# Optimization experiments

Hardware: AMD Instinct MI355X
Metric: run time of the kernel (lower is better)

Reference implementation:

```python
import jax, jax.numpy as jnp
import numpy as np


def setup_inputs() -> dict:
    key = jax.random.key(0)
    k1, k2, k3 = jax.random.split(key, 3)
    B, Cout, Cin, H, W = 8, 64, 64, 256, 256
    Wf_rfft = W // 2 + 1
    init_scale = 0.1
    x = jax.random.normal(k1, (B, Cout, H, W), dtype=jnp.float32)
    weight_fft = jax.random.normal(k2, (Cout, Cin, H, Wf_rfft), dtype=jnp.float32) * init_scale
    bias = jax.random.normal(k3, (Cin,), dtype=jnp.float32) * init_scale
    return {"x": x, "weight_fft": weight_fft, "bias": bias}


def reference(x, weight_fft, bias):
    # x: (B, Cout, H, W); weight_fft: (Cout, Cin, Hf, Wf_rfft); bias: (Cin,)
    B, Cout, H, W = x.shape
    _, Cin, Hf, Wf_rfft = weight_fft.shape
    X_fft = jnp.fft.rfft2(x, axes=(2, 3))  # (B, Cout, H, W//2+1) complex
    # Channel contraction over Cout per frequency bin (original code does a
    # broadcast multiply-then-sum; einsum computes identical math without
    # materializing the (B,Cout,Cin,Hf,Wf) intermediate).
    Z_fft = jnp.einsum('bohw,oihw->bihw', X_fft, weight_fft.astype(X_fft.dtype))
    real_Wf = 2 * (Wf_rfft - 1) if Wf_rfft > 1 else 1
    y = jnp.fft.irfft2(Z_fft, s=(Hf, real_Wf), axes=(2, 3))
    y = y[..., :H, :W]
    return y + bias[None, :, None, None]
```

## Files before the change

kernel.cpp:

```cpp
#include <hip/hip_runtime.h>
#include <hip/hip_bf16.h>
#include <math.h>

#define PI_F 3.14159265358979323846f


#define NWACT 15

__device__ __forceinline__ unsigned pack_bf(float re, float im) {
    unsigned ur = __float_as_uint(re);
    unsigned ui = __float_as_uint(im);
    ur = (ur + 0x7fffu + ((ur >> 16) & 1u)) >> 16;
    ui = (ui + 0x7fffu + ((ui >> 16) & 1u)) & 0xffff0000u;
    return ur | ui;
}
__device__ __forceinline__ float2 unpack_bf(unsigned p) {
    return make_float2(__uint_as_float(p << 16),
                       __uint_as_float(p & 0xffff0000u));
}

__device__ __forceinline__ int s2i(int p) { return p ^ (((p >> 4) & 3) << 2); }

__device__ __forceinline__ float2 cadd(float2 a, float2 b){ return make_float2(a.x+b.x, a.y+b.y); }
__device__ __forceinline__ float2 csub(float2 a, float2 b){ return make_float2(a.x-b.x, a.y-b.y); }
__device__ __forceinline__ float2 cmul(float2 a, float2 b){ return make_float2(a.x*b.x-a.y*b.y, a.x*b.y+a.y*b.x); }

template<int SGN>
__device__ __forceinline__ void mk_tw(int jt, float invh, float2& w1, float2& w2) {
    const float th = (SGN < 0 ? -PI_F : PI_F) * (float)jt * invh;
    __sincosf(th, &w1.y, &w1.x);
    __sincosf(0.5f * th, &w2.y, &w2.x);
}

template<int SGN>
__device__ __forceinline__ void quad2(float2& u0, float2& u1, float2& u2, float2& u3,
                                      float2 w1, float2 w2) {
    const float2 t1 = cmul(w1, u1), t3 = cmul(w1, u3);
    const float2 v0 = cadd(u0, t1), v1 = csub(u0, t1);
    const float2 v2 = cadd(u2, t3), v3 = csub(u2, t3);
    const float2 t2 = cmul(w2, v2);
    float2 t4 = cmul(w2, v3);
    t4 = (SGN < 0) ? make_float2(t4.y, -t4.x) : make_float2(-t4.y, t4.x);
    u0 = cadd(v0, t2); u2 = csub(v0, t2);
    u1 = cadd(v1, t4); u3 = csub(v1, t4);
}

template<int SGN>
__device__ __forceinline__ void fft256(float2* w, int j, const float2* tw,
                                       float2& o0, float2& o1, float2& o2, float2& o3) {
    const int r = (int)(__brev((unsigned)j) >> 26);
    float2 u0 = w[s2i(r)], u1 = w[s2i(r + 128)], u2 = w[s2i(r + 64)], u3 = w[s2i(r + 192)];
    __builtin_amdgcn_wave_barrier();
    {
        const float2 v0 = cadd(u0, u1), v1 = csub(u0, u1);
        const float2 v2 = cadd(u2, u3), v3 = csub(u2, u3);
        const float2 t4 = (SGN < 0) ? make_float2(v3.y, -v3.x) : make_float2(-v3.y, v3.x);
        u0 = cadd(v0, v2); u2 = csub(v0, v2);
        u1 = cadd(v1, t4); u3 = csub(v1, t4);
    }
    const int p4 = s2i(4 * j);
    *(float4*)&w[p4]     = make_float4(u0.x, u0.y, u1.x, u1.y);
    *(float4*)&w[p4 + 2] = make_float4(u2.x, u2.y, u3.x, u3.y);
    __builtin_amdgcn_wave_barrier();
    {
        const int p = ((j >> 2) << 4) | (j & 3);
        float2 a0 = w[s2i(p)], a1 = w[s2i(p+4)], a2 = w[s2i(p+8)], a3 = w[s2i(p+12)];
        quad2<SGN>(a0, a1, a2, a3, tw[0], tw[1]);
        w[s2i(p)] = a0; w[s2i(p+4)] = a1; w[s2i(p+8)] = a2; w[s2i(p+12)] = a3;
    }
    __builtin_amdgcn_wave_barrier();
    {
        const int p = ((j >> 4) << 6) | (j & 15);
        float2 a0 = w[s2i(p)], a1 = w[s2i(p+16)], a2 = w[s2i(p+32)], a3 = w[s2i(p+48)];
        quad2<SGN>(a0, a1, a2, a3, tw[2], tw[3]);
        w[s2i(p)] = a0; w[s2i(p+16)] = a1; w[s2i(p+32)] = a2; w[s2i(p+48)] = a3;
    }
    __builtin_amdgcn_wave_barrier();
    {
        float2 a0 = w[s2i(j)], a1 = w[s2i(j+64)], a2 = w[s2i(j+128)], a3 = w[s2i(j+192)];
        quad2<SGN>(a0, a1, a2, a3, tw[4], tw[5]);
        o0 = a0; o1 = a1; o2 = a2; o3 = a3;
    }
}

#define SMEM_BYTES (132096 + NWACT * 256 * 8)

__global__ __launch_bounds__(1024) void k_fwd2d(const float* __restrict__ x,
                                                unsigned* __restrict__ Xf) {
    extern __shared__ char smem[];
    unsigned* S = (unsigned*)smem;
    float2* w = (float2*)(smem + 132096) + ((threadIdx.x >> 6) << 8);
    const int t = threadIdx.x, f = t >> 6, j = t & 63;
    const int bo = blockIdx.x;
    const float* xi = x + (size_t)bo * 65536;

    float2 tw[6];
    mk_tw<-1>(j & 3,  0.25f,       tw[0], tw[1]);
    mk_tw<-1>(j & 15, 1.0f/16.0f,  tw[2], tw[3]);
    mk_tw<-1>(j,      1.0f/64.0f,  tw[4], tw[5]);

    if (f < NWACT) {
        for (int rp = f; rp < 128; rp += NWACT) {
            const int r1 = rp, r2 = rp + 128;
            const float4 va = ((const float4*)(xi + (r1 << 8)))[j];
            const float4 vb = ((const float4*)(xi + (r2 << 8)))[j];
            const int p4 = s2i(4 * j);
            *(float4*)&w[p4]     = make_float4(va.x, vb.x, va.y, vb.y);
            *(float4*)&w[p4 + 2] = make_float4(va.z, vb.z, va.w, vb.w);
            __builtin_amdgcn_wave_barrier();
            float2 o0, o1, o2, o3;
            fft256<-1>(w, j, tw, o0, o1, o2, o3);
            const int src = (64 - j) & 63;
            float2 P3, P2;
            P3.x = __shfl(o3.x, src); P3.y = __shfl(o3.y, src);
            P2.x = __shfl(o2.x, src); P2.y = __shfl(o2.y, src);
            const float2 Cj = (j == 0) ? make_float2(o0.x, -o0.y)
                                       : make_float2(P3.x, -P3.y);
            const float2 Ck = (j == 0) ? make_float2(P3.x, -P3.y)
                                       : make_float2(P2.x, -P2.y);
            const float2 Aj = make_float2(0.5f * (o0.x + Cj.x), 0.5f * (o0.y + Cj.y));
            const float2 Bj = make_float2(0.5f * (o0.y - Cj.y), -0.5f * (o0.x - Cj.x));
            const float2 Ak = make_float2(0.5f * (o1.x + Ck.x), 0.5f * (o1.y + Ck.y));
            const float2 Bk = make_float2(0.5f * (o1.y - Ck.y), -0.5f * (o1.x - Ck.x));
            S[r1 * 129 + j]      = pack_bf(Aj.x, Aj.y);
            S[r1 * 129 + 64 + j] = pack_bf(Ak.x, Ak.y);
            S[r2 * 129 + j]      = pack_bf(Bj.x, Bj.y);
            S[r2 * 129 + 64 + j] = pack_bf(Bk.x, Bk.y);
            if (j == 0) {
                S[r1 * 129 + 128] = pack_bf(o2.x, 0.0f);
                S[r2 * 129 + 128] = pack_bf(o2.y, 0.0f);
            }
            __builtin_amdgcn_wave_barrier();
        }
    }
    __syncthreads();
    if (f < NWACT) {
        for (int c = f; c <= 128; c += NWACT) {
#pragma unroll
            for (int k = 0; k < 4; ++k)
                w[s2i(j + 64 * k)] = unpack_bf(S[(j + 64 * k) * 129 + c]);
            __builtin_amdgcn_wave_barrier();
            float2 o0, o1, o2, o3;
            fft256<-1>(w, j, tw, o0, o1, o2, o3);
            S[(j      ) * 129 + c] = pack_bf(o0.x, o0.y);
            S[(j +  64) * 129 + c] = pack_bf(o1.x, o1.y);
            S[(j + 128) * 129 + c] = pack_bf(o2.x, o2.y);
            S[(j + 192) * 129 + c] = pack_bf(o3.x, o3.y);
            __builtin_amdgcn_wave_barrier();
        }
    }
    __syncthreads();
    uint4* dst = (uint4*)(Xf + (size_t)bo * 33024);
    const uint4* src4 = (const uint4*)S;
    for (int e = t; e < 8256; e += 1024) dst[e] = src4[e];
}

__global__ __launch_bounds__(256) void k_einsum(unsigned* __restrict__ Xf,
                                                const float* __restrict__ Wt) {
    __shared__ unsigned xs[512][32];
    const int t = threadIdx.x;
    const int bid = blockIdx.x;
    const int nid = (bid & 7) * 129 + (bid >> 3);
    const size_t n0 = (size_t)nid * 32;

#pragma unroll
    for (int k = 0; k < 16; ++k) {
        const int e = t + 256 * k;
        const int pr = e >> 3, q = e & 7;
        const uint4 v = *reinterpret_cast<const uint4*>(
            Xf + (size_t)pr * 33024 + n0 + (q << 2));
        *reinterpret_cast<uint4*>(&xs[pr][q << 2]) = v;
    }
    __syncthreads();

    const int nl = t & 31, j = t >> 5;
    float2 acc[8][8];
#pragma unroll
    for (int r = 0; r < 8; ++r)
#pragma unroll
        for (int b = 0; b < 8; ++b) acc[r][b] = make_float2(0.0f, 0.0f);

    const float* Wb = Wt + n0 + nl;
    auto wload = [&](int o, float (&buf)[8]) {
#pragma unroll
        for (int r = 0; r < 8; ++r)
            buf[r] = __builtin_nontemporal_load(
                Wb + (size_t)((o << 6) | ((r << 3) | j)) * 33024);
    };
    auto fmab = [&](int o, const float (&wc)[8]) {
        float2 xv[8];
#pragma unroll
        for (int b = 0; b < 8; ++b) xv[b] = unpack_bf(xs[(b << 6) | o][nl]);
#pragma unroll
        for (int r = 0; r < 8; ++r)
#pragma unroll
            for (int b = 0; b < 8; ++b) {
                acc[r][b].x += xv[b].x * wc[r];
                acc[r][b].y += xv[b].y * wc[r];
            }
    };

    float wA[8], wB[8];
    wload(0, wA);
    wload(1, wB);
    for (int o = 0; o < 64; o += 2) {
        float wc0[8];
#pragma unroll
        for (int r = 0; r < 8; ++r) wc0[r] = wA[r];
        wload(min(o + 2, 63), wA);
        fmab(o, wc0);
        float wc1[8];
#pragma unroll
        for (int r = 0; r < 8; ++r) wc1[r] = wB[r];
        wload(min(o + 3, 63), wB);
        fmab(o + 1, wc1);
    }

#pragma unroll
    for (int r = 0; r < 8; ++r) {
        const int i = (r << 3) | j;
#pragma unroll
        for (int b = 0; b < 8; ++b) {
            Xf[(size_t)((b << 6) | i) * 33024 + n0 + nl] =
                pack_bf(acc[r][b].x, acc[r][b].y);
        }
    }
}

__global__ __launch_bounds__(1024) void k_inv2d(const unsigned* __restrict__ Xf,
                                                const float* __restrict__ bias,
                                                float* __restrict__ y) {
    extern __shared__ char smem[];
    unsigned* S = (unsigned*)smem;
    float2* w = (float2*)(smem + 132096) + ((threadIdx.x >> 6) << 8);
    const int t = threadIdx.x, f = t >> 6, j = t & 63;
    const int bo = blockIdx.x;
    const float bv = bias[bo & 63];

    float2 tw[6];
    mk_tw<+1>(j & 3,  0.25f,       tw[0], tw[1]);
    mk_tw<+1>(j & 15, 1.0f/16.0f,  tw[2], tw[3]);
    mk_tw<+1>(j,      1.0f/64.0f,  tw[4], tw[5]);

    {
        uint4* s4 = (uint4*)S;
        const uint4* g4 = (const uint4*)(Xf + (size_t)bo * 33024);
        for (int e = t; e < 8256; e += 1024) s4[e] = g4[e];
    }
    __syncthreads();
    if (f < NWACT) {
        for (int c = f; c <= 128; c += NWACT) {
#pragma unroll
            for (int k = 0; k < 4; ++k)
                w[s2i(j + 64 * k)] = unpack_bf(S[(j + 64 * k) * 129 + c]);
            __builtin_amdgcn_wave_barrier();
            float2 o0, o1, o2, o3;
            fft256<+1>(w, j, tw, o0, o1, o2, o3);
            S[(j      ) * 129 + c] = pack_bf(o0.x, o0.y);
            S[(j +  64) * 129 + c] = pack_bf(o1.x, o1.y);
            S[(j + 128) * 129 + c] = pack_bf(o2.x, o2.y);
            S[(j + 192) * 129 + c] = pack_bf(o3.x, o3.y);
            __builtin_amdgcn_wave_barrier();
        }
    }
    __syncthreads();
    float* yo = y + (size_t)bo * 65536;
    if (f < NWACT) {
        for (int rp = f; rp < 128; rp += NWACT) {
            const int r1 = rp, r2 = rp + 128;
            const unsigned* Sa = S + r1 * 129;
            const unsigned* Sb = S + r2 * 129;
            const float2 A0 = unpack_bf(Sa[j]),      B0 = unpack_bf(Sb[j]);
            const float2 A1 = unpack_bf(Sa[j + 64]), B1 = unpack_bf(Sb[j + 64]);
            const int i2 = (j == 0) ? 128 : 128 - j;
            const float2 A2 = unpack_bf(Sa[i2]),     B2 = unpack_bf(Sb[i2]);
            const float2 A3 = unpack_bf(Sa[64 - j]), B3 = unpack_bf(Sb[64 - j]);
            const float2 z0 = (j == 0)
                ? make_float2(A0.x, B0.x)
                : make_float2(A0.x - B0.y, A0.y + B0.x);
            const float2 z1 = make_float2(A1.x - B1.y, A1.y + B1.x);
            const float2 z2 = (j == 0)
                ? make_float2(A2.x, B2.x)
                : make_float2(A2.x + B2.y, B2.x - A2.y);
            const float2 z3 = make_float2(A3.x + B3.y, B3.x - A3.y);
            w[s2i(j)]       = z0;
            w[s2i(j +  64)] = z1;
            w[s2i(j + 128)] = z2;
            w[s2i(j + 192)] = z3;
            __builtin_amdgcn_wave_barrier();
            float2 o0, o1, o2, o3;
            fft256<+1>(w, j, tw, o0, o1, o2, o3);
            const float sc = 1.0f / 65536.0f;
            float* y1 = yo + (r1 << 8);
            float* y2 = yo + (r2 << 8);
            __builtin_nontemporal_store(o0.x * sc + bv, y1 + j);
            __builtin_nontemporal_store(o1.x * sc + bv, y1 + j + 64);
            __builtin_nontemporal_store(o2.x * sc + bv, y1 + j + 128);
            __builtin_nontemporal_store(o3.x * sc + bv, y1 + j + 192);
            __builtin_nontemporal_store(o0.y * sc + bv, y2 + j);
            __builtin_nontemporal_store(o1.y * sc + bv, y2 + j + 64);
            __builtin_nontemporal_store(o2.y * sc + bv, y2 + j + 128);
            __builtin_nontemporal_store(o3.y * sc + bv, y2 + j + 192);
            __builtin_amdgcn_wave_barrier();
        }
    }
}

extern "C" void kernel_launch(void* const* d_in, const int* in_sizes, int n_in,
                              void* d_out, int out_size, void* d_ws,
                              size_t ws_size, hipStream_t stream) {
    (void)in_sizes; (void)n_in; (void)out_size; (void)ws_size;
    const float* x    = (const float*)d_in[0];
    const float* wfft = (const float*)d_in[1];
    const float* bias = (const float*)d_in[2];
    float* y = (float*)d_out;
    unsigned* Xf = (unsigned*)d_ws;

    hipFuncSetAttribute((const void*)k_fwd2d,
                        hipFuncAttributeMaxDynamicSharedMemorySize, SMEM_BYTES);
    hipFuncSetAttribute((const void*)k_inv2d,
                        hipFuncAttributeMaxDynamicSharedMemorySize, SMEM_BYTES);

    k_fwd2d<<<512, 1024, SMEM_BYTES, stream>>>(x, Xf);
    k_einsum<<<1032, 256, 0, stream>>>(Xf, wfft);
    k_inv2d<<<512, 1024, SMEM_BYTES, stream>>>(Xf, bias, y);
}
```

Baseline: 277.0 us.

## Replace column radix-4 FFT256 with in-register 16x16 FFT over four columns per wave

The column pass of both the forward and inverse 2D FFT previously used 15 waves, each running a 64-thread radix-4 FFT256 per column through a per-wave float2 scratch buffer. It now uses all 16 waves, and each wave processes four columns at once with 16 lanes per column. Each lane performs a register-resident 16-point DFT, applies twiddles, exchanges data through the bf16 shared tile using XOR-swizzled indices, and then performs a second 16-point DFT. The goal is fewer wave barriers and scratch round-trips and better wave utilisation. The cost is higher register pressure from 16 complex values per lane, extra twiddle recurrence error, and idle lanes on the final column-128 pass.

```diff
diff --git a/kernel.cpp b/kernel.cpp
--- a/kernel.cpp
+++ b/kernel.cpp
@@ -81,6 +81,81 @@
         quad2<SGN>(a0, a1, a2, a3, tw[4], tw[5]);
         o0 = a0; o1 = a1; o2 = a2; o3 = a3;
     }
+}
+
+template<int SGN>
+__device__ __forceinline__ void dft4(float2& u0, float2& u1, float2& u2, float2& u3) {
+    const float2 t0 = cadd(u0, u2), t1 = csub(u0, u2);
+    const float2 t2 = cadd(u1, u3), t3 = csub(u1, u3);
+    const float2 t3i = (SGN < 0) ? make_float2(t3.y, -t3.x) : make_float2(-t3.y, t3.x);
+    u0 = cadd(t0, t2); u1 = cadd(t1, t3i);
+    u2 = csub(t0, t2); u3 = csub(t1, t3i);
+}
+
+template<int SGN>
+__device__ __forceinline__ void dft16(float2 x[16]) {
+#pragma unroll
+    for (int b = 0; b < 4; ++b) dft4<SGN>(x[b], x[b+4], x[b+8], x[b+12]);
+    const float sg = (SGN < 0) ? -1.0f : 1.0f;
+    const float C8 = 0.9238795325112867f, S8 = 0.3826834323650898f, H = 0.7071067811865476f;
+    x[5]  = cmul(x[5],  make_float2(C8,  sg*S8));
+    x[6]  = cmul(x[6],  make_float2(H,   sg*H));
+    x[7]  = cmul(x[7],  make_float2(S8,  sg*C8));
+    x[9]  = cmul(x[9],  make_float2(H,   sg*H));
+    x[10] = (SGN < 0) ? make_float2(x[10].y, -x[10].x)
+                      : make_float2(-x[10].y, x[10].x);
+    x[11] = cmul(x[11], make_float2(-H,  sg*H));
+    x[13] = cmul(x[13], make_float2(S8,  sg*C8));
+    x[14] = cmul(x[14], make_float2(-H,  sg*H));
+    x[15] = cmul(x[15], make_float2(-C8, -sg*S8));
+#pragma unroll
+    for (int k1 = 0; k1 < 4; ++k1) dft4<SGN>(x[4*k1], x[4*k1+1], x[4*k1+2], x[4*k1+3]);
+}
+
+template<int SGN>
+__device__ __forceinline__ void colfft16(unsigned* __restrict__ S, int l, int c, bool act) {
+    float2 x[16];
+    if (act) {
+#pragma unroll
+        for (int r = 0; r < 16; ++r) x[r] = unpack_bf(S[(16*r + l)*129 + c]);
+    } else {
+#pragma unroll
+        for (int r = 0; r < 16; ++r) x[r] = make_float2(0.0f, 0.0f);
+    }
+    dft16<SGN>(x);
+    float2 twl;
+    {
+        const float th = (SGN < 0 ? -1.0f : 1.0f) * (2.0f * PI_F / 256.0f) * (float)l;
+        __sincosf(th, &twl.y, &twl.x);
+    }
+    float2 t = twl;
+#pragma unroll
+    for (int kk = 1; kk < 16; ++kk) {
+        const int r = 4*(kk & 3) + (kk >> 2);
+        x[r] = cmul(x[r], t);
+        if (kk < 15) t = cmul(t, twl);
+    }
+    if (act) {
+#pragma unroll
+        for (int kk = 0; kk < 16; ++kk) {
+            const int r = 4*(kk & 3) + (kk >> 2);
+            S[(16*kk + (l ^ kk))*129 + c] = pack_bf(x[r].x, x[r].y);
+        }
+    }
+    __builtin_amdgcn_wave_barrier();
+    if (act) {
+#pragma unroll
+        for (int n2 = 0; n2 < 16; ++n2) x[n2] = unpack_bf(S[(16*l + (n2 ^ l))*129 + c]);
+    }
+    dft16<SGN>(x);
+    if (act) {
+#pragma unroll
+        for (int r = 0; r < 16; ++r) {
+            const int kk = 4*(r & 3) + (r >> 2);
+            S[(16*kk + l)*129 + c] = pack_bf(x[r].x, x[r].y);
+        }
+    }
+    __builtin_amdgcn_wave_barrier();
 }
 
 #define SMEM_BYTES (132096 + NWACT * 256 * 8)
@@ -134,19 +209,13 @@
         }
     }
     __syncthreads();
-    if (f < NWACT) {
-        for (int c = f; c <= 128; c += NWACT) {
-#pragma unroll
-            for (int k = 0; k < 4; ++k)
-                w[s2i(j + 64 * k)] = unpack_bf(S[(j + 64 * k) * 129 + c]);
-            __builtin_amdgcn_wave_barrier();
-            float2 o0, o1, o2, o3;
-            fft256<-1>(w, j, tw, o0, o1, o2, o3);
-            S[(j      ) * 129 + c] = pack_bf(o0.x, o0.y);
-            S[(j +  64) * 129 + c] = pack_bf(o1.x, o1.y);
-            S[(j + 128) * 129 + c] = pack_bf(o2.x, o2.y);
-            S[(j + 192) * 129 + c] = pack_bf(o3.x, o3.y);
-            __builtin_amdgcn_wave_barrier();
+    {
+        const int g4 = (t >> 4) & 3, l16 = t & 15;
+        for (int T = f; T < 33; T += 16) {
+            const int cb = (T < 16) ? T : ((T < 32) ? T + 48 : 128);
+            const int c = cb + 16 * g4;
+            const bool act = (T < 32) || (g4 == 0);
+            colfft16<-1>(S, l16, c, act);
         }
     }
     __syncthreads();
@@ -244,23 +313,17 @@
 
     {
         uint4* s4 = (uint4*)S;
-        const uint4* g4 = (const uint4*)(Xf + (size_t)bo * 33024);
-        for (int e = t; e < 8256; e += 1024) s4[e] = g4[e];
-    }
-    __syncthreads();
-    if (f < NWACT) {
-        for (int c = f; c <= 128; c += NWACT) {
-#pragma unroll
-            for (int k = 0; k < 4; ++k)
-                w[s2i(j + 64 * k)] = unpack_bf(S[(j + 64 * k) * 129 + c]);
-            __builtin_amdgcn_wave_barrier();
-            float2 o0, o1, o2, o3;
-            fft256<+1>(w, j, tw, o0, o1, o2, o3);
-            S[(j      ) * 129 + c] = pack_bf(o0.x, o0.y);
-            S[(j +  64) * 129 + c] = pack_bf(o1.x, o1.y);
-            S[(j + 128) * 129 + c] = pack_bf(o2.x, o2.y);
-            S[(j + 192) * 129 + c] = pack_bf(o3.x, o3.y);
-            __builtin_amdgcn_wave_barrier();
+        const uint4* g4p = (const uint4*)(Xf + (size_t)bo * 33024);
+        for (int e = t; e < 8256; e += 1024) s4[e] = g4p[e];
+    }
+    __syncthreads();
+    {
+        const int g4 = (t >> 4) & 3, l16 = t & 15;
+        for (int T = f; T < 33; T += 16) {
+            const int cb = (T < 16) ? T : ((T < 32) ? T + 48 : 128);
+            const int c = cb + 16 * g4;
+            const bool act = (T < 32) || (g4 == 0);
+            colfft16<+1>(S, l16, c, act);
         }
     }
     __syncthreads();
```

Measured after the change: 271.3 us. 1.02x faster.
